# Kernel optimization log

Measured on AMD Instinct MI355X. Metric: run time of the kernel, lower is better.

The kernel has to match this reference:

```python
import jax, jax.numpy as jnp
import numpy as np

BETA = 0.9
THR = 1.0
ALPHA = 2.0  # snntorch surrogate.atan default

@jax.custom_vjp
def atan_spike(x):
    return (x > 0).astype(x.dtype)

def _atan_fwd(x):
    return atan_spike(x), x

def _atan_bwd(x, g):
    # snntorch ATan surrogate: alpha/2 / (1 + (pi/2 * alpha * x)^2)
    return (g * (ALPHA / 2.0) / (1.0 + (jnp.pi / 2.0 * ALPHA * x) ** 2),)

atan_spike.defvjp(_atan_fwd, _atan_bwd)

def setup_inputs() -> dict:
    key = jax.random.key(0)
    k = jax.random.split(key, 5)
    B, T, C, H, W = 128, 25, 3, 64, 64
    F, HID, O = C * H * W, 2048, 2
    bound1 = 1.0 / np.sqrt(F)
    boundo = 1.0 / np.sqrt(HID)
    return {
        "x": jax.random.normal(k[0], (B, T, C, H, W), jnp.float32),
        "W1": jax.random.uniform(k[1], (HID, F), jnp.float32, -bound1, bound1),
        "b1": jax.random.uniform(k[2], (HID,), jnp.float32, -bound1, bound1),
        "Wo": jax.random.uniform(k[3], (O, HID), jnp.float32, -boundo, boundo),
        "bo": jax.random.uniform(k[4], (O,), jnp.float32, -boundo, boundo),
    }

def reference(x, W1, b1, Wo, bo):
    B, T = x.shape[0], x.shape[1]
    HID, O = W1.shape[0], Wo.shape[0]
    xf = x.reshape(B, T, -1).transpose(1, 0, 2)  # [T, B, F]
    # fc1 for all timesteps at once (input is fixed per step)
    h_all = jnp.einsum('tbf,hf->tbh', xf, W1) + b1  # [T, B, HID]

    def step(carry, h):
        mem1, memo = carry
        # snntorch Leaky (reset_mechanism='subtract'): reset from previous mem
        r1 = atan_spike(mem1 - THR)
        mem1 = BETA * mem1 + h - r1 * THR
        s1 = atan_spike(mem1 - THR)
        o = s1 @ Wo.T + bo
        ro = atan_spike(memo - THR)
        memo = BETA * memo + o - ro * THR
        so = atan_spike(memo - THR)
        return (mem1, memo), so

    init = (jnp.zeros((B, HID), x.dtype), jnp.zeros((B, O), x.dtype))
    (_, _), spk_rec = jax.lax.scan(step, init, h_all)
    # train=False path: sum of output spikes over time
    return spk_rec.sum(axis=0)  # [B, O]
```

## Files before the change

### kernel.cpp

```cpp
#include <hip/hip_runtime.h>


#define T_STEPS 25
#define B_SZ    128
#define F_SZ    12288
#define HID_SZ  2048
#define KT      384
#define M_PAD   3328
#define PART_STRIDE ((size_t)M_PAD * HID_SZ)

typedef __attribute__((ext_vector_type(8))) _Float16 f16x8;
typedef __attribute__((ext_vector_type(4))) float f32x4;
typedef __attribute__((ext_vector_type(16))) float f32x16;

__device__ __forceinline__ void g2l16(const void* g, void* l) {
  __builtin_amdgcn_global_load_lds(
      (const __attribute__((address_space(1))) void*)g,
      (__attribute__((address_space(3))) void*)l, 16, 0, 0);
}

__global__ __launch_bounds__(256) void conv_x_kernel(
    const float* __restrict__ x, char* __restrict__ A2) {
  const int total = 13 * KT * 256 * 4;
  for (int i = blockIdx.x * 256 + threadIdx.x; i < total; i += gridDim.x * 256) {
    const int s = i & 3;
    const int r = (i >> 2) & 255;
    const int mtkt = i >> 10;
    const int kt = mtkt % KT;
    const int m = (mtkt / KT) * 256 + r;
    const int b = m & 127;
    const int t = m >> 7;
    f16x8 hi = {0, 0, 0, 0, 0, 0, 0, 0};
    f16x8 lo = {0, 0, 0, 0, 0, 0, 0, 0};
    if (t < T_STEPS) {
      const float* src = x + ((size_t)(b * T_STEPS + t)) * F_SZ + kt * 32 + s * 8;
      float4 v0 = *(const float4*)src;
      float4 v1 = *(const float4*)(src + 4);
      float vf[8] = {v0.x, v0.y, v0.z, v0.w, v1.x, v1.y, v1.z, v1.w};
#pragma unroll
      for (int j = 0; j < 8; ++j) {
        _Float16 h = (_Float16)vf[j];
        hi[j] = h;
        lo[j] = (_Float16)(vf[j] - (float)h);
      }
    }
    char* chunk = A2 + (size_t)mtkt * 32768;
    *(f16x8*)(chunk + s * 4096 + r * 16) = hi;
    *(f16x8*)(chunk + (s + 4) * 4096 + r * 16) = lo;
  }
}

__global__ __launch_bounds__(256) void conv_w_kernel(
    const float* __restrict__ W1, char* __restrict__ B2) {
  const int total = 8 * KT * 256 * 4;
  for (int i = blockIdx.x * 256 + threadIdx.x; i < total; i += gridDim.x * 256) {
    const int s = i & 3;
    const int c = (i >> 2) & 255;
    const int ntkt = i >> 10;
    const int kt = ntkt % KT;
    const int n = (ntkt / KT) * 256 + c;
    const float* src = W1 + (size_t)n * F_SZ + kt * 32 + s * 8;
    float4 v0 = *(const float4*)src;
    float4 v1 = *(const float4*)(src + 4);
    float vf[8] = {v0.x, v0.y, v0.z, v0.w, v1.x, v1.y, v1.z, v1.w};
    f16x8 hi, lo;
#pragma unroll
    for (int j = 0; j < 8; ++j) {
      float vs = vf[j] * 128.0f;
      _Float16 h = (_Float16)vs;
      hi[j] = h;
      lo[j] = (_Float16)(vs - (float)h);
    }
    char* chunk = B2 + (size_t)ntkt * 32768;
    *(f16x8*)(chunk + s * 4096 + c * 16) = hi;
    *(f16x8*)(chunk + (s + 4) * 4096 + c * 16) = lo;
  }
}

__global__ __launch_bounds__(512, 1) void gemm_tile_kernel(
    const char* __restrict__ A2, const char* __restrict__ B2,
    float* __restrict__ parts) {
  __shared__ __align__(16) char lds[131072];
  const int tid = threadIdx.x;
  const int l = tid & 63;
  const int w = tid >> 6;
  const int wm = w >> 2;
  const int wn = w & 3;
  const int lhalf = l >> 5;

  const int swz = (blockIdx.x & 7) * 26 + (blockIdx.x >> 3);
  const int sp = swz & 1;
  const int mnt = swz >> 1;
  const int mt = mnt >> 3;
  const int nt = mnt & 7;
  const int kt0 = sp * 192;
  const int ktN = kt0 + 192;

  const char* aC = A2 + (size_t)mt * KT * 32768;
  const char* bC = B2 + (size_t)nt * KT * 32768;
  const int arow = (wm * 128 + (l & 31)) * 16;
  const int brow = (wn * 64 + (l & 31)) * 16;

#define STAGE(ktx, buf)                                                  \
  do {                                                                   \
    char* d_ = (char*)lds + (buf) * 65536 + tid * 16;                    \
    const char* a_ = aC + (size_t)(ktx) * 32768 + tid * 16;              \
    const char* b_ = bC + (size_t)(ktx) * 32768 + tid * 16;              \
    g2l16(a_, d_);                 g2l16(a_ + 8192, d_ + 8192);          \
    g2l16(a_ + 16384, d_ + 16384); g2l16(a_ + 24576, d_ + 24576);        \
    g2l16(b_, d_ + 32768);         g2l16(b_ + 8192, d_ + 40960);         \
    g2l16(b_ + 16384, d_ + 49152); g2l16(b_ + 24576, d_ + 57344);        \
  } while (0)

  f32x16 acc[4][2];
#pragma unroll
  for (int i = 0; i < 4; ++i)
#pragma unroll
    for (int j = 0; j < 2; ++j)
#pragma unroll
      for (int r = 0; r < 16; ++r) acc[i][j][r] = 0.f;

  STAGE(kt0, 0);
  int buf = 0;

  for (int kt = kt0; kt < ktN; ++kt) {
    __syncthreads();
    if (kt + 1 < ktN) STAGE(kt + 1, buf ^ 1);

    const char* la = (const char*)lds + buf * 65536;
    const char* lb = la + 32768;

#pragma unroll
    for (int ks = 0; ks < 2; ++ks) {
      const int g = ks * 2 + lhalf;
      f16x8 ah[4], al[4], bh[2], bl[2];
#pragma unroll
      for (int mf = 0; mf < 4; ++mf) {
        ah[mf] = *(const f16x8*)(la + g * 4096 + arow + mf * 512);
        al[mf] = *(const f16x8*)(la + (g + 4) * 4096 + arow + mf * 512);
      }
#pragma unroll
      for (int nf = 0; nf < 2; ++nf) {
        bh[nf] = *(const f16x8*)(lb + g * 4096 + brow + nf * 512);
        bl[nf] = *(const f16x8*)(lb + (g + 4) * 4096 + brow + nf * 512);
      }
      __builtin_amdgcn_s_setprio(1);
#pragma unroll
      for (int mf = 0; mf < 4; ++mf)
#pragma unroll
        for (int nf = 0; nf < 2; ++nf) {
          acc[mf][nf] = __builtin_amdgcn_mfma_f32_32x32x16_f16(ah[mf], bh[nf], acc[mf][nf], 0, 0, 0);
          acc[mf][nf] = __builtin_amdgcn_mfma_f32_32x32x16_f16(ah[mf], bl[nf], acc[mf][nf], 0, 0, 0);
          acc[mf][nf] = __builtin_amdgcn_mfma_f32_32x32x16_f16(al[mf], bh[nf], acc[mf][nf], 0, 0, 0);
        }
      __builtin_amdgcn_s_setprio(0);
    }
    buf ^= 1;
  }

  float* dst = parts + (size_t)sp * PART_STRIDE;
  const int row0 = mt * 256 + wm * 128 + (lhalf << 2);
  const int col0 = nt * 256 + wn * 64 + (l & 31);
#pragma unroll
  for (int nf = 0; nf < 2; ++nf)
#pragma unroll
    for (int mf = 0; mf < 4; ++mf)
#pragma unroll
      for (int r = 0; r < 16; ++r) {
        const int row = row0 + mf * 32 + (r & 3) + ((r >> 2) << 3);
        dst[(size_t)row * HID_SZ + col0 + nf * 32] = acc[mf][nf][r];
      }
#undef STAGE
}

__global__ __launch_bounds__(256) void gemm_h_kernel(
    const float* __restrict__ x, const float* __restrict__ W1,
    const float* __restrict__ b1, float* __restrict__ h_all) {
  __shared__ float As[16][128];
  __shared__ float Bs[16][128];
  const int tid = threadIdx.x;
  const int tx = tid & 15;
  const int ty = tid >> 4;
  const int m0 = blockIdx.x * 128;
  const int n0 = blockIdx.y * 128;
  const int lrow = tid >> 1;
  const int lcol = (tid & 1) * 8;
  const int gm = m0 + lrow;
  const int bb = gm & (B_SZ - 1);
  const int tt = gm >> 7;
  const float* aptr = x + ((size_t)bb * T_STEPS + tt) * F_SZ + lcol;
  const float* bptr = W1 + (size_t)(n0 + lrow) * F_SZ + lcol;
  float acc[8][8];
#pragma unroll
  for (int i = 0; i < 8; ++i)
#pragma unroll
    for (int j = 0; j < 8; ++j) acc[i][j] = 0.f;
  for (int k0 = 0; k0 < F_SZ; k0 += 16) {
    float4 av0 = *(const float4*)(aptr + k0);
    float4 av1 = *(const float4*)(aptr + k0 + 4);
    float4 bv0 = *(const float4*)(bptr + k0);
    float4 bv1 = *(const float4*)(bptr + k0 + 4);
    As[lcol + 0][lrow] = av0.x; As[lcol + 1][lrow] = av0.y;
    As[lcol + 2][lrow] = av0.z; As[lcol + 3][lrow] = av0.w;
    As[lcol + 4][lrow] = av1.x; As[lcol + 5][lrow] = av1.y;
    As[lcol + 6][lrow] = av1.z; As[lcol + 7][lrow] = av1.w;
    Bs[lcol + 0][lrow] = bv0.x; Bs[lcol + 1][lrow] = bv0.y;
    Bs[lcol + 2][lrow] = bv0.z; Bs[lcol + 3][lrow] = bv0.w;
    Bs[lcol + 4][lrow] = bv1.x; Bs[lcol + 5][lrow] = bv1.y;
    Bs[lcol + 6][lrow] = bv1.z; Bs[lcol + 7][lrow] = bv1.w;
    __syncthreads();
#pragma unroll
    for (int k = 0; k < 16; ++k) {
      float4 a0 = *(const float4*)&As[k][ty * 8];
      float4 a1 = *(const float4*)&As[k][ty * 8 + 4];
      float4 q0 = *(const float4*)&Bs[k][tx * 8];
      float4 q1 = *(const float4*)&Bs[k][tx * 8 + 4];
      float ar[8] = {a0.x, a0.y, a0.z, a0.w, a1.x, a1.y, a1.z, a1.w};
      float br[8] = {q0.x, q0.y, q0.z, q0.w, q1.x, q1.y, q1.z, q1.w};
#pragma unroll
      for (int i = 0; i < 8; ++i)
#pragma unroll
        for (int j = 0; j < 8; ++j)
          acc[i][j] = fmaf(ar[i], br[j], acc[i][j]);
    }
    __syncthreads();
  }
#pragma unroll
  for (int i = 0; i < 8; ++i) {
    const int gm2 = m0 + ty * 8 + i;
    float* orow = h_all + (size_t)gm2 * HID_SZ + n0 + tx * 8;
    const float* brow = b1 + n0 + tx * 8;
#pragma unroll
    for (int j = 0; j < 8; ++j) orow[j] = acc[i][j] + brow[j];
  }
}

__global__ __launch_bounds__(256) void lif_hidden_kernel(
    const float* __restrict__ parts, const float* __restrict__ b1,
    const float* __restrict__ Wo, float* __restrict__ oc, int mode) {
  const int b = blockIdx.x & 127;
  const int half = blockIdx.x >> 7;
  const int tid = threadIdx.x;
  const int h0 = half * 1024;
  float mem1[4], wo0[4], wo1[4], bv[4];
#pragma unroll
  for (int i = 0; i < 4; ++i) {
    const int hid = h0 + 256 * i + tid;
    mem1[i] = 0.f;
    wo0[i] = Wo[hid];
    wo1[i] = Wo[HID_SZ + hid];
    bv[i] = b1[hid];
  }
  __shared__ float partial[4][2];
  for (int t = 0; t < T_STEPS; ++t) {
    const int row = t * B_SZ + b;
    const size_t rowb = (size_t)row * HID_SZ;
    float pr0 = 0.f, pr1 = 0.f;
#pragma unroll
    for (int i = 0; i < 4; ++i) {
      const int hid = h0 + 256 * i + tid;
      const size_t idx = rowb + hid;
      float h;
      if (mode == 1) {
        float s = parts[idx] + parts[idx + PART_STRIDE];
        h = s * 0.0078125f + bv[i];
      } else {
        h = parts[idx];
      }
      float r1 = mem1[i] > 1.0f ? 1.0f : 0.0f;
      float m = 0.9f * mem1[i] + h - r1;
      mem1[i] = m;
      if (m > 1.0f) { pr0 += wo0[i]; pr1 += wo1[i]; }
    }
#pragma unroll
    for (int off = 32; off > 0; off >>= 1) {
      pr0 += __shfl_down(pr0, off);
      pr1 += __shfl_down(pr1, off);
    }
    if ((tid & 63) == 0) { partial[tid >> 6][0] = pr0; partial[tid >> 6][1] = pr1; }
    __syncthreads();
    if (tid == 0) {
      const size_t o = (((size_t)b * 2 + half) * T_STEPS + t) * 2;
      oc[o + 0] = partial[0][0] + partial[1][0] + partial[2][0] + partial[3][0];
      oc[o + 1] = partial[0][1] + partial[1][1] + partial[2][1] + partial[3][1];
    }
    __syncthreads();
  }
}

__global__ __launch_bounds__(128) void lif_out_kernel(
    const float* __restrict__ oc, const float* __restrict__ bo,
    float* __restrict__ out) {
  const int b = threadIdx.x;
  float memo0 = 0.f, memo1 = 0.f, a0 = 0.f, a1 = 0.f;
  const float bo0 = bo[0], bo1 = bo[1];
  for (int t = 0; t < T_STEPS; ++t) {
    const size_t i0 = (((size_t)b * 2 + 0) * T_STEPS + t) * 2;
    const size_t i1 = (((size_t)b * 2 + 1) * T_STEPS + t) * 2;
    float o0 = oc[i0] + oc[i1] + bo0;
    float o1 = oc[i0 + 1] + oc[i1 + 1] + bo1;
    float ro0 = memo0 > 1.0f ? 1.0f : 0.0f;
    float ro1 = memo1 > 1.0f ? 1.0f : 0.0f;
    memo0 = 0.9f * memo0 + o0 - ro0;
    memo1 = 0.9f * memo1 + o1 - ro1;
    a0 += memo0 > 1.0f ? 1.0f : 0.0f;
    a1 += memo1 > 1.0f ? 1.0f : 0.0f;
  }
  out[b * 2 + 0] = a0;
  out[b * 2 + 1] = a1;
}

extern "C" void kernel_launch(void* const* d_in, const int* in_sizes, int n_in,
                              void* d_out, int out_size, void* d_ws, size_t ws_size,
                              hipStream_t stream) {
  const float* x  = (const float*)d_in[0];
  const float* W1 = (const float*)d_in[1];
  const float* b1 = (const float*)d_in[2];
  const float* Wo = (const float*)d_in[3];
  const float* bo = (const float*)d_in[4];
  float* out = (float*)d_out;

  const size_t part_bytes = PART_STRIDE * 4;
  const size_t a2_bytes = (size_t)13 * KT * 32768;
  const size_t b2_bytes = (size_t)8 * KT * 32768;
  const size_t oc_bytes = (size_t)128 * 2 * T_STEPS * 2 * 4;
  char* ws = (char*)d_ws;
  float* parts = (float*)ws;

  if (ws_size >= 2 * part_bytes + a2_bytes + b2_bytes + oc_bytes) {
    char* A2 = ws + 2 * part_bytes;
    char* B2 = A2 + a2_bytes;
    float* oc = (float*)(B2 + b2_bytes);
    conv_x_kernel<<<2048, 256, 0, stream>>>(x, A2);
    conv_w_kernel<<<2048, 256, 0, stream>>>(W1, B2);
    gemm_tile_kernel<<<208, 512, 0, stream>>>(A2, B2, parts);
    lif_hidden_kernel<<<256, 256, 0, stream>>>(parts, b1, Wo, oc, 1);
    lif_out_kernel<<<1, 128, 0, stream>>>(oc, bo, out);
  } else {
    float* oc = (float*)(ws + part_bytes);
    dim3 grid(25, 16);
    gemm_h_kernel<<<grid, 256, 0, stream>>>(x, W1, b1, (float*)ws);
    lif_hidden_kernel<<<256, 256, 0, stream>>>((const float*)ws, b1, Wo, oc, 0);
    lif_out_kernel<<<1, 128, 0, stream>>>(oc, bo, out);
  }
}
```

Baseline: 567.4 us.

## Use stream-K persistent GEMM over 256 CUs with multi-slot partial reduction

```diff
diff --git a/kernel.cpp b/kernel.cpp
--- a/kernel.cpp
+++ b/kernel.cpp
@@ -7,6 +7,7 @@
 #define HID_SZ  2048
 #define KT      384
 #define M_PAD   3328
+#define UPB     156
 #define PART_STRIDE ((size_t)M_PAD * HID_SZ)
 
 typedef __attribute__((ext_vector_type(8))) _Float16 f16x8;
@@ -77,7 +78,7 @@
   }
 }
 
-__global__ __launch_bounds__(512, 1) void gemm_tile_kernel(
+__global__ __launch_bounds__(512, 1) void gemm_persist_kernel(
     const char* __restrict__ A2, const char* __restrict__ B2,
     float* __restrict__ parts) {
   __shared__ __align__(16) char lds[131072];
@@ -88,89 +89,129 @@
   const int wn = w & 3;
   const int lhalf = l >> 5;
 
-  const int swz = (blockIdx.x & 7) * 26 + (blockIdx.x >> 3);
-  const int sp = swz & 1;
-  const int mnt = swz >> 1;
-  const int mt = mnt >> 3;
-  const int nt = mnt & 7;
-  const int kt0 = sp * 192;
-  const int ktN = kt0 + 192;
-
-  const char* aC = A2 + (size_t)mt * KT * 32768;
-  const char* bC = B2 + (size_t)nt * KT * 32768;
+  const int swz = ((blockIdx.x & 7) << 5) + (blockIdx.x >> 3);
+
   const int arow = (wm * 128 + (l & 31)) * 16;
   const int brow = (wn * 64 + (l & 31)) * 16;
 
+  int u = swz * UPB;
+  const int u1 = u + UPB;
+
+  while (u < u1) {
+    const int mnt = u / 384;
+    const int kt0 = u - mnt * 384;
+    const int rem_t = 384 - kt0, rem_u = u1 - u;
+    const int seg = rem_t < rem_u ? rem_t : rem_u;
+    const int ktN = kt0 + seg;
+    const int mt = mnt >> 3;
+    const int nt = mnt & 7;
+
+    const char* aC = A2 + (size_t)mt * KT * 32768;
+    const char* bC = B2 + (size_t)nt * KT * 32768;
+
 #define STAGE(ktx, buf)                                                  \
-  do {                                                                   \
-    char* d_ = (char*)lds + (buf) * 65536 + tid * 16;                    \
-    const char* a_ = aC + (size_t)(ktx) * 32768 + tid * 16;              \
-    const char* b_ = bC + (size_t)(ktx) * 32768 + tid * 16;              \
-    g2l16(a_, d_);                 g2l16(a_ + 8192, d_ + 8192);          \
-    g2l16(a_ + 16384, d_ + 16384); g2l16(a_ + 24576, d_ + 24576);        \
-    g2l16(b_, d_ + 32768);         g2l16(b_ + 8192, d_ + 40960);         \
-    g2l16(b_ + 16384, d_ + 49152); g2l16(b_ + 24576, d_ + 57344);        \
-  } while (0)
-
-  f32x16 acc[4][2];
-#pragma unroll
-  for (int i = 0; i < 4; ++i)
-#pragma unroll
-    for (int j = 0; j < 2; ++j)
-#pragma unroll
-      for (int r = 0; r < 16; ++r) acc[i][j][r] = 0.f;
-
-  STAGE(kt0, 0);
-  int buf = 0;
-
-  for (int kt = kt0; kt < ktN; ++kt) {
-    __syncthreads();
-    if (kt + 1 < ktN) STAGE(kt + 1, buf ^ 1);
-
-    const char* la = (const char*)lds + buf * 65536;
-    const char* lb = la + 32768;
-
-#pragma unroll
-    for (int ks = 0; ks < 2; ++ks) {
-      const int g = ks * 2 + lhalf;
-      f16x8 ah[4], al[4], bh[2], bl[2];
+    do {                                                                 \
+      char* d_ = (char*)lds + (buf) * 65536 + tid * 16;                  \
+      const char* a_ = aC + (size_t)(ktx) * 32768 + tid * 16;            \
+      const char* b_ = bC + (size_t)(ktx) * 32768 + tid * 16;            \
+      g2l16(a_, d_);                 g2l16(a_ + 8192, d_ + 8192);        \
+      g2l16(a_ + 16384, d_ + 16384); g2l16(a_ + 24576, d_ + 24576);      \
+      g2l16(b_, d_ + 32768);         g2l16(b_ + 8192, d_ + 40960);       \
+      g2l16(b_ + 16384, d_ + 49152); g2l16(b_ + 24576, d_ + 57344);      \
+    } while (0)
+
+    f32x16 acc[4][2];
+#pragma unroll
+    for (int i = 0; i < 4; ++i)
+#pragma unroll
+      for (int j = 0; j < 2; ++j)
+#pragma unroll
+        for (int r = 0; r < 16; ++r) acc[i][j][r] = 0.f;
+
+    STAGE(kt0, 0);
+    int buf = 0;
+
+    for (int kt = kt0; kt < ktN; ++kt) {
+      __syncthreads();
+      const int ktpf = (kt + 1 < ktN) ? kt + 1 : kt;
+      STAGE(ktpf, buf ^ 1);
+
+      const char* la = (const char*)lds + buf * 65536;
+      const char* lb = la + 32768;
+      const int g0 = lhalf;
+      const int g1 = 2 + lhalf;
+
+      f16x8 ah0[4], al0[4], bh0[2], bl0[2];
+      f16x8 ah1[4], al1[4], bh1[2], bl1[2];
 #pragma unroll
       for (int mf = 0; mf < 4; ++mf) {
-        ah[mf] = *(const f16x8*)(la + g * 4096 + arow + mf * 512);
-        al[mf] = *(const f16x8*)(la + (g + 4) * 4096 + arow + mf * 512);
+        ah0[mf] = *(const f16x8*)(la + g0 * 4096 + arow + mf * 512);
+        al0[mf] = *(const f16x8*)(la + (g0 + 4) * 4096 + arow + mf * 512);
       }
 #pragma unroll
       for (int nf = 0; nf < 2; ++nf) {
-        bh[nf] = *(const f16x8*)(lb + g * 4096 + brow + nf * 512);
-        bl[nf] = *(const f16x8*)(lb + (g + 4) * 4096 + brow + nf * 512);
-      }
+        bh0[nf] = *(const f16x8*)(lb + g0 * 4096 + brow + nf * 512);
+        bl0[nf] = *(const f16x8*)(lb + (g0 + 4) * 4096 + brow + nf * 512);
+      }
+#pragma unroll
+      for (int mf = 0; mf < 4; ++mf) {
+        ah1[mf] = *(const f16x8*)(la + g1 * 4096 + arow + mf * 512);
+        al1[mf] = *(const f16x8*)(la + (g1 + 4) * 4096 + arow + mf * 512);
+      }
+#pragma unroll
+      for (int nf = 0; nf < 2; ++nf) {
+        bh1[nf] = *(const f16x8*)(lb + g1 * 4096 + brow + nf * 512);
+        bl1[nf] = *(const f16x8*)(lb + (g1 + 4) * 4096 + brow + nf * 512);
+      }
+
       __builtin_amdgcn_s_setprio(1);
 #pragma unroll
       for (int mf = 0; mf < 4; ++mf)
 #pragma unroll
         for (int nf = 0; nf < 2; ++nf) {
-          acc[mf][nf] = __builtin_amdgcn_mfma_f32_32x32x16_f16(ah[mf], bh[nf], acc[mf][nf], 0, 0, 0);
-          acc[mf][nf] = __builtin_amdgcn_mfma_f32_32x32x16_f16(ah[mf], bl[nf], acc[mf][nf], 0, 0, 0);
-          acc[mf][nf] = __builtin_amdgcn_mfma_f32_32x32x16_f16(al[mf], bh[nf], acc[mf][nf], 0, 0, 0);
+          acc[mf][nf] = __builtin_amdgcn_mfma_f32_32x32x16_f16(ah0[mf], bh0[nf], acc[mf][nf], 0, 0, 0);
+          acc[mf][nf] = __builtin_amdgcn_mfma_f32_32x32x16_f16(ah0[mf], bl0[nf], acc[mf][nf], 0, 0, 0);
+          acc[mf][nf] = __builtin_amdgcn_mfma_f32_32x32x16_f16(al0[mf], bh0[nf], acc[mf][nf], 0, 0, 0);
+        }
+#pragma unroll
+      for (int mf = 0; mf < 4; ++mf)
+#pragma unroll
+        for (int nf = 0; nf < 2; ++nf) {
+          acc[mf][nf] = __builtin_amdgcn_mfma_f32_32x32x16_f16(ah1[mf], bh1[nf], acc[mf][nf], 0, 0, 0);
+          acc[mf][nf] = __builtin_amdgcn_mfma_f32_32x32x16_f16(ah1[mf], bl1[nf], acc[mf][nf], 0, 0, 0);
+          acc[mf][nf] = __builtin_amdgcn_mfma_f32_32x32x16_f16(al1[mf], bh1[nf], acc[mf][nf], 0, 0, 0);
         }
       __builtin_amdgcn_s_setprio(0);
-    }
-    buf ^= 1;
-  }
-
-  float* dst = parts + (size_t)sp * PART_STRIDE;
-  const int row0 = mt * 256 + wm * 128 + (lhalf << 2);
-  const int col0 = nt * 256 + wn * 64 + (l & 31);
-#pragma unroll
-  for (int nf = 0; nf < 2; ++nf)
-#pragma unroll
-    for (int mf = 0; mf < 4; ++mf)
-#pragma unroll
-      for (int r = 0; r < 16; ++r) {
-        const int row = row0 + mf * 32 + (r & 3) + ((r >> 2) << 3);
-        dst[(size_t)row * HID_SZ + col0 + nf * 32] = acc[mf][nf][r];
-      }
+
+      __builtin_amdgcn_sched_group_barrier(0x010, 8, 0);
+      __builtin_amdgcn_sched_group_barrier(0x100, 12, 0);
+#pragma unroll
+      for (int i = 0; i < 12; ++i) {
+        __builtin_amdgcn_sched_group_barrier(0x008, 2, 0);
+        __builtin_amdgcn_sched_group_barrier(0x100, 1, 0);
+      }
+      __builtin_amdgcn_sched_group_barrier(0x008, 24, 0);
+
+      buf ^= 1;
+    }
+
+    const int slot = swz - (mnt * 384) / UPB;
+    float* dst = parts + (size_t)slot * PART_STRIDE;
+    const int row0 = mt * 256 + wm * 128 + (lhalf << 2);
+    const int col0 = nt * 256 + wn * 64 + (l & 31);
+#pragma unroll
+    for (int nf = 0; nf < 2; ++nf)
+#pragma unroll
+      for (int mf = 0; mf < 4; ++mf)
+#pragma unroll
+        for (int r = 0; r < 16; ++r) {
+          const int row = row0 + mf * 32 + (r & 3) + ((r >> 2) << 3);
+          dst[(size_t)row * HID_SZ + col0 + nf * 32] = acc[mf][nf][r];
+        }
+    u += seg;
+    __syncthreads();
 #undef STAGE
+  }
 }
 
 __global__ __launch_bounds__(256) void gemm_h_kernel(
@@ -255,14 +296,19 @@
   for (int t = 0; t < T_STEPS; ++t) {
     const int row = t * B_SZ + b;
     const size_t rowb = (size_t)row * HID_SZ;
+    const int mt8 = (row >> 8) * 8;
     float pr0 = 0.f, pr1 = 0.f;
 #pragma unroll
     for (int i = 0; i < 4; ++i) {
       const int hid = h0 + 256 * i + tid;
       const size_t idx = rowb + hid;
       float h;
-      if (mode == 1) {
-        float s = parts[idx] + parts[idx + PART_STRIDE];
+      if (mode == 2) {
+        float s = parts[idx] + parts[idx + PART_STRIDE] +
+                  parts[idx + 2 * PART_STRIDE];
+        const int k0 = (mt8 + (hid >> 8)) * 384;
+        if ((k0 + 383) / UPB - k0 / UPB + 1 == 4)
+          s += parts[idx + 3 * PART_STRIDE];
         h = s * 0.0078125f + bv[i];
       } else {
         h = parts[idx];
@@ -327,14 +373,14 @@
   char* ws = (char*)d_ws;
   float* parts = (float*)ws;
 
-  if (ws_size >= 2 * part_bytes + a2_bytes + b2_bytes + oc_bytes) {
-    char* A2 = ws + 2 * part_bytes;
+  if (ws_size >= 4 * part_bytes + a2_bytes + b2_bytes + oc_bytes) {
+    char* A2 = ws + 4 * part_bytes;
     char* B2 = A2 + a2_bytes;
     float* oc = (float*)(B2 + b2_bytes);
     conv_x_kernel<<<2048, 256, 0, stream>>>(x, A2);
     conv_w_kernel<<<2048, 256, 0, stream>>>(W1, B2);
-    gemm_tile_kernel<<<208, 512, 0, stream>>>(A2, B2, parts);
-    lif_hidden_kernel<<<256, 256, 0, stream>>>(parts, b1, Wo, oc, 1);
+    gemm_persist_kernel<<<256, 512, 0, stream>>>(A2, B2, parts);
+    lif_hidden_kernel<<<256, 256, 0, stream>>>(parts, b1, Wo, oc, 2);
     lif_out_kernel<<<1, 128, 0, stream>>>(oc, bo, out);
   } else {
     float* oc = (float*)(ws + part_bytes);
```

Measured after the change: 580.6 us. +2.3%, slower.
